# Performance work log

Hardware: AMD Instinct MI355X
Metric: run time of the kernel (lower is better)

## Reference

```python
import jax, jax.numpy as jnp
import numpy as np

R = 4  # num_relations
G = 256  # num graphs in batch


def rgcn_conv(x, W, root, b, src, dst, etype, num_nodes):
    # PyG RGCNConv (default aggr='mean'):
    # out_i = root @ x_i + b + sum_r mean_{j in N_r(i)} W_r @ x_j
    xr = jnp.einsum('ni,rio->rno', x, W)            # [R, N, O]
    m = xr[etype, src]                               # [E, O] per-edge messages
    seg = dst * R + etype                            # (node, relation) segment id
    ones = jnp.ones(etype.shape, dtype=x.dtype)
    cnt = jax.ops.segment_sum(ones, seg, num_segments=num_nodes * R)
    norm = 1.0 / jnp.maximum(cnt[seg], 1.0)          # 1/|N_r(i)| per edge
    agg = jax.ops.segment_sum(m * norm[:, None], dst, num_segments=num_nodes)
    return agg + x @ root + b


def forward(x, W1, root1, b1, W2, root2, b2, W3, root3, b3,
            Wf1, bf1, Wh, bh, Wl, bl, src, dst, etype, batch):
    N = x.shape[0]
    h = jax.nn.relu(rgcn_conv(x, W1, root1, b1, src, dst, etype, N))
    h = jax.nn.relu(rgcn_conv(h, W2, root2, b2, src, dst, etype, N))
    h = rgcn_conv(h, W3, root3, b3, src, dst, etype, N)        # [N, 64]
    g = jax.ops.segment_max(h, batch, num_segments=G)          # scatter_max pool [G, 64]
    # MLP head: 64 -> 128 -> 256 -> num_classes, ReLU, softmax(dim=1)
    g = jax.nn.relu(g @ Wf1 + bf1)
    g = jax.nn.relu(g @ Wh + bh)
    g = g @ Wl + bl
    return jax.nn.softmax(g, axis=1)


def setup_inputs() -> dict:
    key = jax.random.key(0)
    ks = jax.random.split(key, 20)
    N, E, num_classes = 100000, 1600000, 51

    def glorot(k, shape):
        fan_in, fan_out = shape[-2], shape[-1]
        s = jnp.sqrt(6.0 / (fan_in + fan_out))
        return jax.random.uniform(k, shape, jnp.float32, -s, s)

    x = jax.random.normal(ks[0], (N, 16), jnp.float32)
    edge_index = jax.random.randint(ks[1], (2, E), 0, N)
    edge_type = jax.random.randint(ks[2], (E,), 0, R)
    batch = (jnp.arange(N) * G) // N  # sorted, covers all G graphs

    inp = {
        'x': x, 'edge_index': edge_index, 'edge_type': edge_type, 'batch': batch,
        'W1': glorot(ks[3], (R, 16, 16)), 'root1': glorot(ks[4], (16, 16)), 'b1': jnp.zeros((16,)),
        'W2': glorot(ks[5], (R, 16, 32)), 'root2': glorot(ks[6], (16, 32)), 'b2': jnp.zeros((32,)),
        'W3': glorot(ks[7], (R, 32, 64)), 'root3': glorot(ks[8], (32, 64)), 'b3': jnp.zeros((64,)),
        'Wf1': glorot(ks[9], (64, 128)), 'bf1': jnp.zeros((128,)),
        'Wh': glorot(ks[10], (128, 256)), 'bh': jnp.zeros((256,)),
        'Wl': glorot(ks[11], (256, num_classes)), 'bl': jnp.zeros((num_classes,)),
    }
    return inp


def reference(x, W1, root1, b1, W2, root2, b2, W3, root3, b3,
              Wf1, bf1, Wh, bh, Wl, bl, edge_index, edge_type, batch):
    src, dst = edge_index[0], edge_index[1]
    return forward(x, W1, root1, b1, W2, root2, b2, W3, root3, b3,
                   Wf1, bf1, Wh, bh, Wl, bl, src, dst, etype=edge_type, batch=batch)
```

## Files before the change

### kernel.cpp

```cpp
#include <hip/hip_runtime.h>

#define RELS 4
#define NGRAPH 256
#define SCAN_BLK 2048

static inline size_t alignup(size_t x) { return (x + 255) & ~(size_t)255; }

__global__ void hist_kernel(const int* __restrict__ dst, const int* __restrict__ et,
                            int* __restrict__ hcnt, int E)
{
    int e = blockIdx.x * blockDim.x + threadIdx.x;
    if (e < E) atomicAdd(&hcnt[dst[e] * RELS + et[e]], 1);
}

__global__ __launch_bounds__(256)
void scan1_kernel(const int* __restrict__ in, int* __restrict__ excl,
                  int* __restrict__ bsum, int n)
{
    __shared__ int lds[256];
    int tid = threadIdx.x;
    int base = blockIdx.x * SCAN_BLK + tid * 8;
    int v[8];
    #pragma unroll
    for (int i = 0; i < 8; ++i) v[i] = (base + i < n) ? in[base + i] : 0;
    int run = 0;
    #pragma unroll
    for (int i = 0; i < 8; ++i) { int t = v[i]; v[i] = run; run += t; }
    lds[tid] = run;
    __syncthreads();
    for (int off = 1; off < 256; off <<= 1) {
        int t = (tid >= off) ? lds[tid - off] : 0;
        __syncthreads();
        lds[tid] += t;
        __syncthreads();
    }
    int ex = (tid > 0) ? lds[tid - 1] : 0;
    if (tid == 255) bsum[blockIdx.x] = lds[255];
    #pragma unroll
    for (int i = 0; i < 8; ++i) if (base + i < n) excl[base + i] = v[i] + ex;
}

__global__ __launch_bounds__(256)
void scan2_kernel(const int* __restrict__ bsum, int* __restrict__ boff, int nb)
{
    __shared__ int lds[256];
    int tid = threadIdx.x;
    lds[tid] = (tid < nb) ? bsum[tid] : 0;
    __syncthreads();
    for (int off = 1; off < 256; off <<= 1) {
        int t = (tid >= off) ? lds[tid - off] : 0;
        __syncthreads();
        lds[tid] += t;
        __syncthreads();
    }
    if (tid < nb) boff[tid] = (tid > 0) ? lds[tid - 1] : 0;
}

__global__ void scan3_kernel(const int* __restrict__ excl, const int* __restrict__ boff,
                             int* __restrict__ ptr, int n, int total)
{
    int i = blockIdx.x * blockDim.x + threadIdx.x;
    if (i < n) ptr[i] = excl[i] + boff[i / SCAN_BLK];
    if (i == 0) ptr[n] = total;
}

__global__ void fill_kernel(const int* __restrict__ src, const int* __restrict__ dst,
                            const int* __restrict__ et, const int* __restrict__ ptr,
                            int* __restrict__ cursor, int* __restrict__ ssrc, int E)
{
    int e = blockIdx.x * blockDim.x + threadIdx.x;
    if (e < E) {
        int seg = dst[e] * RELS + et[e];
        int pos = atomicAdd(&cursor[seg], 1);
        ssrc[ptr[seg] + pos] = src[e];
    }
}

template<int IN, int OUT, bool RELU, int MINW>
__global__ __launch_bounds__(256, MINW)
void rgcn_layer_kernel(const float* __restrict__ feat,
                       const int* __restrict__ ptr, const int* __restrict__ ssrc,
                       const float* __restrict__ W, const float* __restrict__ root,
                       const float* __restrict__ bias,
                       float* __restrict__ hout, int n)
{
    constexpr int NPB  = 64;
    constexpr int K    = 4 * IN;
    constexpr int AGS  = K + 1;
    constexpr int NF4  = IN / 16;
    constexpr int LPN4 = IN / 4;
    constexpr int Q    = OUT / 4;

    __shared__ float agg[NPB * AGS];

    const int tid  = (int)threadIdx.x;
    const int nl   = tid >> 2;
    const int c4   = tid & 3;
    const int node = (int)blockIdx.x * NPB + nl;

    const float4* fv = (const float4*)feat;

    if (node < n) {
        int4 p4  = *(const int4*)(ptr + (size_t)node * RELS);
        int pend = ptr[(size_t)node * RELS + RELS];
        int pb[RELS + 1] = {p4.x, p4.y, p4.z, p4.w, pend};
        float* arow = &agg[nl * AGS];

        #pragma unroll
        for (int r = 0; r < RELS; ++r) {
            float4 ac[NF4];
            #pragma unroll
            for (int j = 0; j < NF4; ++j) ac[j] = {0.f, 0.f, 0.f, 0.f};
            int p0 = pb[r], p1 = pb[r + 1];
            int e = p0;
            for (; e + 4 <= p1; e += 4) {
                int s0 = ssrc[e], s1 = ssrc[e + 1], s2 = ssrc[e + 2], s3 = ssrc[e + 3];
                #pragma unroll
                for (int j = 0; j < NF4; ++j) {
                    float4 v0 = fv[(size_t)s0 * LPN4 + c4 + 4 * j];
                    float4 v1 = fv[(size_t)s1 * LPN4 + c4 + 4 * j];
                    float4 v2 = fv[(size_t)s2 * LPN4 + c4 + 4 * j];
                    float4 v3 = fv[(size_t)s3 * LPN4 + c4 + 4 * j];
                    ac[j].x += (v0.x + v1.x) + (v2.x + v3.x);
                    ac[j].y += (v0.y + v1.y) + (v2.y + v3.y);
                    ac[j].z += (v0.z + v1.z) + (v2.z + v3.z);
                    ac[j].w += (v0.w + v1.w) + (v2.w + v3.w);
                }
            }
            for (; e < p1; ++e) {
                int sn = ssrc[e];
                #pragma unroll
                for (int j = 0; j < NF4; ++j) {
                    float4 v = fv[(size_t)sn * LPN4 + c4 + 4 * j];
                    ac[j].x += v.x; ac[j].y += v.y; ac[j].z += v.z; ac[j].w += v.w;
                }
            }
            float nm = 1.0f / fmaxf((float)(p1 - p0), 1.0f);
            #pragma unroll
            for (int j = 0; j < NF4; ++j) {
                int kb = r * IN + (c4 + 4 * j) * 4;
                arow[kb + 0] = ac[j].x * nm;
                arow[kb + 1] = ac[j].y * nm;
                arow[kb + 2] = ac[j].z * nm;
                arow[kb + 3] = ac[j].w * nm;
            }
        }
    }
    __syncthreads();

    const int qw   = __builtin_amdgcn_readfirstlane(tid >> 6);
    const int lane = tid & 63;
    const int cn   = (int)blockIdx.x * NPB + lane;
    const int cnc  = (cn < n) ? cn : (n - 1);

    const float* __restrict__ wq = W    + qw * Q;
    const float* __restrict__ rq = root + qw * Q;
    const float* __restrict__ bq = bias + qw * Q;
    const float* arow = &agg[lane * AGS];

    float4 own[LPN4];
    #pragma unroll
    for (int j = 0; j < LPN4; ++j) own[j] = fv[(size_t)cnc * LPN4 + j];

    float acc[Q];
    #pragma unroll
    for (int o = 0; o < Q; ++o) acc[o] = bq[o];

    #pragma unroll 4
    for (int k = 0; k < K; ++k) {
        float m = arow[k];
        const float* wr = wq + (size_t)k * OUT;
        #pragma unroll
        for (int o = 0; o < Q; ++o) acc[o] += m * wr[o];
    }
    #pragma unroll
    for (int j = 0; j < LPN4; ++j) {
        #pragma unroll
        for (int c = 0; c < 4; ++c) {
            float m = (&own[j].x)[c];
            const float* wr = rq + (size_t)(j * 4 + c) * OUT;
            #pragma unroll
            for (int o = 0; o < Q; ++o) acc[o] += m * wr[o];
        }
    }

    if (cn < n) {
        float* ho = hout + (size_t)cn * OUT + qw * Q;
        #pragma unroll
        for (int o = 0; o < Q; o += 4) {
            float4 v;
            v.x = RELU ? fmaxf(acc[o + 0], 0.f) : acc[o + 0];
            v.y = RELU ? fmaxf(acc[o + 1], 0.f) : acc[o + 1];
            v.z = RELU ? fmaxf(acc[o + 2], 0.f) : acc[o + 2];
            v.w = RELU ? fmaxf(acc[o + 3], 0.f) : acc[o + 3];
            *(float4*)(ho + o) = v;
        }
    }
}

__device__ inline int lower_bound_i(const int* a, int n, int key)
{
    int lo = 0, hi = n;
    while (lo < hi) { int mid = (lo + hi) >> 1; if (a[mid] < key) lo = mid + 1; else hi = mid; }
    return lo;
}

__global__ __launch_bounds__(256)
void pool_kernel(const float* __restrict__ h3, const int* __restrict__ batch,
                 float* __restrict__ gpool, int n)
{
    int g = blockIdx.x;
    int t = threadIdx.x;
    int ch = t & 63, q = t >> 6;

    int start = lower_bound_i(batch, n, g);
    int end   = lower_bound_i(batch, n, g + 1);

    float m = -INFINITY;
    for (int r = start + q; r < end; r += 4)
        m = fmaxf(m, h3[(size_t)r * 64 + ch]);

    __shared__ float red[4][64];
    red[q][ch] = m;
    __syncthreads();
    if (q == 0) {
        m = fmaxf(fmaxf(red[0][ch], red[1][ch]), fmaxf(red[2][ch], red[3][ch]));
        gpool[g * 64 + ch] = m;
    }
}

__global__ __launch_bounds__(256)
void mlp_kernel(const float* __restrict__ gpool,
                const float* __restrict__ Wf1, const float* __restrict__ bf1,
                const float* __restrict__ Wh,  const float* __restrict__ bh,
                const float* __restrict__ Wl,  const float* __restrict__ bl,
                float* __restrict__ out)
{
    __shared__ float gin[64];
    __shared__ float f1[128];
    __shared__ float f2[256];
    __shared__ float lg[51];
    int g = blockIdx.x, t = threadIdx.x;

    if (t < 64) gin[t] = gpool[g * 64 + t];
    __syncthreads();

    if (t < 128) {
        float a = bf1[t];
        #pragma unroll 8
        for (int k = 0; k < 64; ++k) a += gin[k] * Wf1[k * 128 + t];
        f1[t] = fmaxf(a, 0.f);
    }
    __syncthreads();

    {
        float a = bh[t];
        #pragma unroll 8
        for (int k = 0; k < 128; ++k) a += f1[k] * Wh[k * 256 + t];
        f2[t] = fmaxf(a, 0.f);
    }
    __syncthreads();

    if (t < 51) {
        float a = bl[t];
        #pragma unroll 8
        for (int k = 0; k < 256; ++k) a += f2[k] * Wl[k * 51 + t];
        lg[t] = a;
    }
    __syncthreads();

    if (t == 0) {
        float m = lg[0];
        for (int i = 1; i < 51; ++i) m = fmaxf(m, lg[i]);
        float ssum = 0.f;
        for (int i = 0; i < 51; ++i) { float e = __expf(lg[i] - m); lg[i] = e; ssum += e; }
        float inv = 1.0f / ssum;
        for (int i = 0; i < 51; ++i) out[g * 51 + i] = lg[i] * inv;
    }
}

extern "C" void kernel_launch(void* const* d_in, const int* in_sizes, int n_in,
                              void* d_out, int out_size, void* d_ws, size_t ws_size,
                              hipStream_t stream)
{
    const float* x    = (const float*)d_in[0];
    const int*   ei   = (const int*)d_in[1];
    const int*   et   = (const int*)d_in[2];
    const int*   batch= (const int*)d_in[3];
    const float* W1   = (const float*)d_in[4];
    const float* r1   = (const float*)d_in[5];
    const float* b1   = (const float*)d_in[6];
    const float* W2   = (const float*)d_in[7];
    const float* r2   = (const float*)d_in[8];
    const float* b2   = (const float*)d_in[9];
    const float* W3   = (const float*)d_in[10];
    const float* r3   = (const float*)d_in[11];
    const float* b3   = (const float*)d_in[12];
    const float* Wf1  = (const float*)d_in[13];
    const float* bf1  = (const float*)d_in[14];
    const float* Wh   = (const float*)d_in[15];
    const float* bh   = (const float*)d_in[16];
    const float* Wl   = (const float*)d_in[17];
    const float* bl   = (const float*)d_in[18];

    const int N = in_sizes[0] / 16;
    const int E = in_sizes[2];
    const int NSEG = N * RELS;
    const int NBLK = (NSEG + SCAN_BLK - 1) / SCAN_BLK;
    const int* srcp = ei;
    const int* dstp = ei + E;

    char* ws = (char*)d_ws;
    size_t off = 0;
    int*   hcnt   = (int*)(ws + off);   off += alignup((size_t)NSEG * 4);
    int*   ptr    = (int*)(ws + off);   off += alignup((size_t)(NSEG + 1) * 4);
    int*   excl   = (int*)(ws + off);   off += alignup((size_t)NSEG * 4);
    int*   bsum   = (int*)(ws + off);   off += alignup(256 * 4);
    int*   boff   = (int*)(ws + off);   off += alignup(256 * 4);
    int*   cursor = (int*)(ws + off);   off += alignup((size_t)NSEG * 4);
    int*   ssrc   = (int*)(ws + off);   off += alignup((size_t)E * 4);
    float* h1     = (float*)(ws + off); off += alignup((size_t)N * 16 * 4);
    float* h2     = (float*)(ws + off); off += alignup((size_t)N * 32 * 4);
    float* h3     = (float*)(ws + off); off += alignup((size_t)N * 64 * 4);
    float* gpool  = (float*)(ws + off); off += alignup((size_t)NGRAPH * 64 * 4);
    (void)ws_size; (void)n_in; (void)out_size;

    (void)hipMemsetAsync(hcnt, 0, (size_t)NSEG * 4, stream);
    (void)hipMemsetAsync(cursor, 0, (size_t)NSEG * 4, stream);
    hist_kernel<<<(E + 255) / 256, 256, 0, stream>>>(dstp, et, hcnt, E);
    scan1_kernel<<<NBLK, 256, 0, stream>>>(hcnt, excl, bsum, NSEG);
    scan2_kernel<<<1, 256, 0, stream>>>(bsum, boff, NBLK);
    scan3_kernel<<<(NSEG + 255) / 256, 256, 0, stream>>>(excl, boff, ptr, NSEG, E);
    fill_kernel<<<(E + 255) / 256, 256, 0, stream>>>(srcp, dstp, et, ptr, cursor, ssrc, E);

    rgcn_layer_kernel<16, 16, true, 8><<<(N + 63) / 64, 256, 0, stream>>>(
        x, ptr, ssrc, W1, r1, b1, h1, N);
    rgcn_layer_kernel<16, 32, true, 8><<<(N + 63) / 64, 256, 0, stream>>>(
        h1, ptr, ssrc, W2, r2, b2, h2, N);
    rgcn_layer_kernel<32, 64, false, 4><<<(N + 63) / 64, 256, 0, stream>>>(
        h2, ptr, ssrc, W3, r3, b3, h3, N);

    pool_kernel<<<NGRAPH, 256, 0, stream>>>(h3, batch, gpool, N);

    mlp_kernel<<<NGRAPH, 256, 0, stream>>>(gpool, Wf1, bf1, Wh, bh, Wl, bl, (float*)d_out);
}
```

Before: 326.3 us.

## Widen lanes per node in RGCN gather and seed fill cursor from scan

The layer kernel now uses 512-thread blocks with one float4 slice per lane, so the third layer gets 8 lanes per node instead of 4. The dense phase splits output columns across more waves, and the own-feature load moves inside the loop. The CSR fill seeds cursor with ptr in scan3, which drops a memset and the ptr reload, and it writes ssrc with nontemporal stores. This is meant to raise memory-level parallelism in the gather and trim preprocessing traffic, at the cost of larger blocks, more register and LDS pressure per block, and a changed occupancy hint.

```diff
diff --git a/kernel.cpp b/kernel.cpp
--- a/kernel.cpp
+++ b/kernel.cpp
@@ -57,45 +57,53 @@
 }
 
 __global__ void scan3_kernel(const int* __restrict__ excl, const int* __restrict__ boff,
-                             int* __restrict__ ptr, int n, int total)
+                             int* __restrict__ ptr, int* __restrict__ cursor,
+                             int n, int total)
 {
     int i = blockIdx.x * blockDim.x + threadIdx.x;
-    if (i < n) ptr[i] = excl[i] + boff[i / SCAN_BLK];
+    if (i < n) {
+        int v = excl[i] + boff[i / SCAN_BLK];
+        ptr[i] = v;
+        cursor[i] = v;
+    }
     if (i == 0) ptr[n] = total;
 }
 
 __global__ void fill_kernel(const int* __restrict__ src, const int* __restrict__ dst,
-                            const int* __restrict__ et, const int* __restrict__ ptr,
+                            const int* __restrict__ et,
                             int* __restrict__ cursor, int* __restrict__ ssrc, int E)
 {
     int e = blockIdx.x * blockDim.x + threadIdx.x;
     if (e < E) {
         int seg = dst[e] * RELS + et[e];
         int pos = atomicAdd(&cursor[seg], 1);
-        ssrc[ptr[seg] + pos] = src[e];
-    }
-}
-
-template<int IN, int OUT, bool RELU, int MINW>
-__global__ __launch_bounds__(256, MINW)
+        __builtin_nontemporal_store(src[e], &ssrc[pos]);
+    }
+}
+
+template<int IN, int OUT, bool RELU, int LPN, int MINW>
+__global__ __launch_bounds__(512, MINW)
 void rgcn_layer_kernel(const float* __restrict__ feat,
                        const int* __restrict__ ptr, const int* __restrict__ ssrc,
                        const float* __restrict__ W, const float* __restrict__ root,
                        const float* __restrict__ bias,
                        float* __restrict__ hout, int n)
 {
-    constexpr int NPB  = 64;
-    constexpr int K    = 4 * IN;
-    constexpr int AGS  = K + 1;
-    constexpr int NF4  = IN / 16;
-    constexpr int LPN4 = IN / 4;
-    constexpr int Q    = OUT / 4;
+    constexpr int TPB = 512;
+    constexpr int NPB = TPB / LPN;
+    constexpr int K   = 4 * IN;
+    constexpr int AGS = K + 1;
+    constexpr int F4  = IN / 4;
+    constexpr int Q   = OUT / LPN;
+    constexpr int NB  = NPB / 64;
+
+    static_assert(F4 == LPN, "one float4 slice per lane");
 
     __shared__ float agg[NPB * AGS];
 
     const int tid  = (int)threadIdx.x;
-    const int nl   = tid >> 2;
-    const int c4   = tid & 3;
+    const int nl   = tid / LPN;
+    const int c4   = tid % LPN;
     const int node = (int)blockIdx.x * NPB + nl;
 
     const float4* fv = (const float4*)feat;
@@ -108,59 +116,47 @@
 
         #pragma unroll
         for (int r = 0; r < RELS; ++r) {
-            float4 ac[NF4];
-            #pragma unroll
-            for (int j = 0; j < NF4; ++j) ac[j] = {0.f, 0.f, 0.f, 0.f};
+            float4 ac = {0.f, 0.f, 0.f, 0.f};
             int p0 = pb[r], p1 = pb[r + 1];
             int e = p0;
             for (; e + 4 <= p1; e += 4) {
                 int s0 = ssrc[e], s1 = ssrc[e + 1], s2 = ssrc[e + 2], s3 = ssrc[e + 3];
-                #pragma unroll
-                for (int j = 0; j < NF4; ++j) {
-                    float4 v0 = fv[(size_t)s0 * LPN4 + c4 + 4 * j];
-                    float4 v1 = fv[(size_t)s1 * LPN4 + c4 + 4 * j];
-                    float4 v2 = fv[(size_t)s2 * LPN4 + c4 + 4 * j];
-                    float4 v3 = fv[(size_t)s3 * LPN4 + c4 + 4 * j];
-                    ac[j].x += (v0.x + v1.x) + (v2.x + v3.x);
-                    ac[j].y += (v0.y + v1.y) + (v2.y + v3.y);
-                    ac[j].z += (v0.z + v1.z) + (v2.z + v3.z);
-                    ac[j].w += (v0.w + v1.w) + (v2.w + v3.w);
-                }
+                float4 v0 = fv[(size_t)s0 * F4 + c4];
+                float4 v1 = fv[(size_t)s1 * F4 + c4];
+                float4 v2 = fv[(size_t)s2 * F4 + c4];
+                float4 v3 = fv[(size_t)s3 * F4 + c4];
+                ac.x += (v0.x + v1.x) + (v2.x + v3.x);
+                ac.y += (v0.y + v1.y) + (v2.y + v3.y);
+                ac.z += (v0.z + v1.z) + (v2.z + v3.z);
+                ac.w += (v0.w + v1.w) + (v2.w + v3.w);
             }
             for (; e < p1; ++e) {
                 int sn = ssrc[e];
-                #pragma unroll
-                for (int j = 0; j < NF4; ++j) {
-                    float4 v = fv[(size_t)sn * LPN4 + c4 + 4 * j];
-                    ac[j].x += v.x; ac[j].y += v.y; ac[j].z += v.z; ac[j].w += v.w;
-                }
+                float4 v = fv[(size_t)sn * F4 + c4];
+                ac.x += v.x; ac.y += v.y; ac.z += v.z; ac.w += v.w;
             }
             float nm = 1.0f / fmaxf((float)(p1 - p0), 1.0f);
-            #pragma unroll
-            for (int j = 0; j < NF4; ++j) {
-                int kb = r * IN + (c4 + 4 * j) * 4;
-                arow[kb + 0] = ac[j].x * nm;
-                arow[kb + 1] = ac[j].y * nm;
-                arow[kb + 2] = ac[j].z * nm;
-                arow[kb + 3] = ac[j].w * nm;
-            }
+            int kb = r * IN + c4 * 4;
+            arow[kb + 0] = ac.x * nm;
+            arow[kb + 1] = ac.y * nm;
+            arow[kb + 2] = ac.z * nm;
+            arow[kb + 3] = ac.w * nm;
         }
     }
     __syncthreads();
 
-    const int qw   = __builtin_amdgcn_readfirstlane(tid >> 6);
+    const int wv   = __builtin_amdgcn_readfirstlane(tid >> 6);
     const int lane = tid & 63;
-    const int cn   = (int)blockIdx.x * NPB + lane;
+    const int nb   = wv % NB;
+    const int cg   = wv / NB;
+    const int ln   = nb * 64 + lane;
+    const int cn   = (int)blockIdx.x * NPB + ln;
     const int cnc  = (cn < n) ? cn : (n - 1);
 
-    const float* __restrict__ wq = W    + qw * Q;
-    const float* __restrict__ rq = root + qw * Q;
-    const float* __restrict__ bq = bias + qw * Q;
-    const float* arow = &agg[lane * AGS];
-
-    float4 own[LPN4];
-    #pragma unroll
-    for (int j = 0; j < LPN4; ++j) own[j] = fv[(size_t)cnc * LPN4 + j];
+    const float* __restrict__ wq = W    + cg * Q;
+    const float* __restrict__ rq = root + cg * Q;
+    const float* __restrict__ bq = bias + cg * Q;
+    const float* arow = &agg[ln * AGS];
 
     float acc[Q];
     #pragma unroll
@@ -174,10 +170,11 @@
         for (int o = 0; o < Q; ++o) acc[o] += m * wr[o];
     }
     #pragma unroll
-    for (int j = 0; j < LPN4; ++j) {
+    for (int j = 0; j < F4; ++j) {
+        float4 v = fv[(size_t)cnc * F4 + j];
         #pragma unroll
         for (int c = 0; c < 4; ++c) {
-            float m = (&own[j].x)[c];
+            float m = (&v.x)[c];
             const float* wr = rq + (size_t)(j * 4 + c) * OUT;
             #pragma unroll
             for (int o = 0; o < Q; ++o) acc[o] += m * wr[o];
@@ -185,7 +182,7 @@
     }
 
     if (cn < n) {
-        float* ho = hout + (size_t)cn * OUT + qw * Q;
+        float* ho = hout + (size_t)cn * OUT + cg * Q;
         #pragma unroll
         for (int o = 0; o < Q; o += 4) {
             float4 v;
@@ -326,18 +323,17 @@
     (void)ws_size; (void)n_in; (void)out_size;
 
     (void)hipMemsetAsync(hcnt, 0, (size_t)NSEG * 4, stream);
-    (void)hipMemsetAsync(cursor, 0, (size_t)NSEG * 4, stream);
     hist_kernel<<<(E + 255) / 256, 256, 0, stream>>>(dstp, et, hcnt, E);
     scan1_kernel<<<NBLK, 256, 0, stream>>>(hcnt, excl, bsum, NSEG);
     scan2_kernel<<<1, 256, 0, stream>>>(bsum, boff, NBLK);
-    scan3_kernel<<<(NSEG + 255) / 256, 256, 0, stream>>>(excl, boff, ptr, NSEG, E);
-    fill_kernel<<<(E + 255) / 256, 256, 0, stream>>>(srcp, dstp, et, ptr, cursor, ssrc, E);
-
-    rgcn_layer_kernel<16, 16, true, 8><<<(N + 63) / 64, 256, 0, stream>>>(
+    scan3_kernel<<<(NSEG + 255) / 256, 256, 0, stream>>>(excl, boff, ptr, cursor, NSEG, E);
+    fill_kernel<<<(E + 255) / 256, 256, 0, stream>>>(srcp, dstp, et, cursor, ssrc, E);
+
+    rgcn_layer_kernel<16, 16, true, 4, 8><<<(N + 127) / 128, 512, 0, stream>>>(
         x, ptr, ssrc, W1, r1, b1, h1, N);
-    rgcn_layer_kernel<16, 32, true, 8><<<(N + 63) / 64, 256, 0, stream>>>(
+    rgcn_layer_kernel<16, 32, true, 4, 8><<<(N + 127) / 128, 512, 0, stream>>>(
         h1, ptr, ssrc, W2, r2, b2, h2, N);
-    rgcn_layer_kernel<32, 64, false, 4><<<(N + 63) / 64, 256, 0, stream>>>(
+    rgcn_layer_kernel<32, 64, false, 8, 8><<<(N + 63) / 64, 512, 0, stream>>>(
         h2, ptr, ssrc, W3, r3, b3, h3, N);
 
     pool_kernel<<<NGRAPH, 256, 0, stream>>>(h3, batch, gpool, N);
```

After: 365.8 us. 12.1% more time.
